# Optimization experiments

Measured on AMD Instinct MI355X. Metric: run time of the kernel, lower is better.

Reference implementation:

```python
import jax, jax.numpy as jnp
import numpy as np


def setup_inputs() -> dict:
    key = jax.random.key(0)
    k1, k2, k3, k4, k5 = jax.random.split(key, 5)
    B, N, T, O, G = 32, 256, 1024, 1024, 8
    x = jax.random.normal(k1, (B, N, T), dtype=jnp.float32)
    y = jax.random.uniform(k2, (B, G), dtype=jnp.float32)  # genre mixture weights
    weight = jax.random.normal(k3, (G, O, T), dtype=jnp.float32) * (1.0 / np.sqrt(T))
    mask = jax.random.uniform(k4, (O, T), dtype=jnp.float32)
    bias = jax.random.normal(k5, (O,), dtype=jnp.float32)
    return {"x": x, "y": y, "weight": weight, "mask": mask, "bias": bias}


def reference(x, y, weight, mask, bias):
    # mask the shared weight bank: [G,O,T] * [1,O,T]
    masked_w = weight * mask[None, :, :]
    # per-sample genre-mixed weights: [B,G] x [G,O,T] -> [B,O,T]
    w_bot = jnp.einsum('bg,got->bot', y, masked_w)
    # batched masked linear: [B,N,T] x [B,O,T] -> [B,N,O], plus bias
    return jnp.einsum('bnt,bot->bno', x, w_bot) + bias
```

## Files before the change

### kernel.cpp

```cpp
#include <hip/hip_runtime.h>
#include <hip/hip_bf16.h>
#include <stdint.h>


#define B_ 32
#define N_ 256
#define T_ 1024
#define O_ 1024
#define G_ 8

#define WSTRIDE ((size_t)(O_ * T_ + 2048))

#define BM 128
#define BN 128
#define BK 64
#define BUFSZ (BM * BK)

typedef __attribute__((__ext_vector_type__(8)))  __bf16 bf16x8;
typedef __attribute__((__ext_vector_type__(16))) float  f32x16;

__device__ __forceinline__ unsigned short f2bf(float f) {
    union { float f; uint32_t u; } v; v.f = f;
    uint32_t u = v.u;
    uint32_t r = (u + 0x7fffu + ((u >> 16) & 1u)) >> 16;
    return (unsigned short)r;
}

__device__ __forceinline__ uint4 pack8(const float* a) {
    uint4 r;
    r.x = (uint32_t)f2bf(a[0]) | ((uint32_t)f2bf(a[1]) << 16);
    r.y = (uint32_t)f2bf(a[2]) | ((uint32_t)f2bf(a[3]) << 16);
    r.z = (uint32_t)f2bf(a[4]) | ((uint32_t)f2bf(a[5]) << 16);
    r.w = (uint32_t)f2bf(a[6]) | ((uint32_t)f2bf(a[7]) << 16);
    return r;
}

#define MIXB 1024
#define CVTB 1024

__global__ __launch_bounds__(256) void prep_kernel(
    const float* __restrict__ w,
    const float* __restrict__ mask,
    const float* __restrict__ y,
    const float* __restrict__ x,
    unsigned short* __restrict__ Wb,
    unsigned short* __restrict__ xb)
{
    const int tid = threadIdx.x;
    if (blockIdx.x < MIXB) {
        const int idx = blockIdx.x * 256 + tid;
        const int o   = idx >> 8;
        const int t   = (idx & 255) << 2;

        const float4 m4 = *(const float4*)(mask + (size_t)o * T_ + t);

        float wv[G_][4];
#pragma unroll
        for (int g = 0; g < G_; ++g) {
            const float4 a = *(const float4*)(w + ((size_t)g * O_ + o) * T_ + t);
            wv[g][0] = a.x * m4.x; wv[g][1] = a.y * m4.y;
            wv[g][2] = a.z * m4.z; wv[g][3] = a.w * m4.w;
        }
        unsigned short* dst = Wb + (size_t)o * T_ + t;
        const int bph = blockIdx.x & (B_ - 1);
#pragma unroll 4
        for (int bi = 0; bi < B_; ++bi) {
            const int b = (bi + bph) & (B_ - 1);
            const float4 y0 = *(const float4*)(y + b * G_);
            const float4 y1 = *(const float4*)(y + b * G_ + 4);
            const float yv[G_] = {y0.x, y0.y, y0.z, y0.w, y1.x, y1.y, y1.z, y1.w};
            float acc[4] = {};
#pragma unroll
            for (int g = 0; g < G_; ++g)
#pragma unroll
                for (int j = 0; j < 4; ++j)
                    acc[j] += yv[g] * wv[g][j];
            ushort4 pk;
            pk.x = f2bf(acc[0]); pk.y = f2bf(acc[1]);
            pk.z = f2bf(acc[2]); pk.w = f2bf(acc[3]);
            *(ushort4*)(dst + (size_t)b * WSTRIDE) = pk;
        }
    } else {
        const int i = (blockIdx.x - MIXB) * 256 + tid;
        const float4* x4 = (const float4*)x;
        uint4* o4 = (uint4*)xb;
#pragma unroll
        for (int j = 0; j < 4; ++j) {
            const size_t f4 = (size_t)j * 524288 + (size_t)i * 2;
            const float4 a = x4[f4];
            const float4 b = x4[f4 + 1];
            const float v[8] = {a.x, a.y, a.z, a.w, b.x, b.y, b.z, b.w};
            o4[(size_t)j * 262144 + i] = pack8(v);
        }
    }
}

__device__ __forceinline__ void load16_to_lds(const unsigned short* g, unsigned short* l) {
    __builtin_amdgcn_global_load_lds(
        (const __attribute__((address_space(1))) unsigned char*)g,
        (__attribute__((address_space(3))) unsigned char*)l,
        16, 0, 0);
}

__global__ __launch_bounds__(256, 2) void gemm_kernel(
    const unsigned short* __restrict__ xb,
    const unsigned short* __restrict__ Wb,
    const float* __restrict__ bias,
    float* __restrict__ out)
{
    __shared__ __align__(16) unsigned short lA[2 * BUFSZ];
    __shared__ __align__(16) unsigned short lB[2 * BUFSZ];

    const int tn = blockIdx.x;
    const int tm = blockIdx.y;
    const int b  = blockIdx.z;

    const int tid  = threadIdx.x;
    const int lane = tid & 63;
    const int wave = tid >> 6;
    const int wm   = (wave >> 1) * 64;
    const int wn   = (wave & 1) * 64;

    const unsigned short* Ab = xb + (size_t)b * N_ * T_ + (size_t)(tm * BM) * T_;
    const unsigned short* Bb = Wb + (size_t)b * WSTRIDE + (size_t)(tn * BN) * T_;

    const int srow   = tid >> 3;
    const int schunk = (tid & 7) ^ (srow & 7);
    const unsigned short* ga0 = Ab + (size_t)srow * T_ + schunk * 8;
    const unsigned short* gb0 = Bb + (size_t)srow * T_ + schunk * 8;

#define STAGE(buf, kt)                                                          \
    {                                                                           \
        unsigned short* lad = lA + (buf) * BUFSZ + tid * 8;                     \
        unsigned short* lbd = lB + (buf) * BUFSZ + tid * 8;                     \
        _Pragma("unroll")                                                       \
        for (int i_ = 0; i_ < 4; ++i_) {                                        \
            load16_to_lds(ga0 + (kt) + (size_t)(i_ * 32) * T_, lad + i_ * 2048);\
            load16_to_lds(gb0 + (kt) + (size_t)(i_ * 32) * T_, lbd + i_ * 2048);\
        }                                                                       \
    }

    f32x16 acc[2][2] = {};

    const int fr   = lane & 31;
    const int half = lane >> 5;
    const int sw   = fr & 7;

#define COMPUTE(buf)                                                            \
    {                                                                           \
        const unsigned short* la = lA + (buf) * BUFSZ;                          \
        const unsigned short* lb = lB + (buf) * BUFSZ;                          \
        _Pragma("unroll")                                                       \
        for (int ks = 0; ks < 4; ++ks) {                                        \
            const int cp = (((ks * 2 + half)) ^ sw) * 8;                        \
            bf16x8 afr[2], bfr[2];                                              \
            _Pragma("unroll")                                                   \
            for (int i_ = 0; i_ < 2; ++i_)                                      \
                afr[i_] = *(const bf16x8*)(la + (wm + i_ * 32 + fr) * BK + cp); \
            _Pragma("unroll")                                                   \
            for (int i_ = 0; i_ < 2; ++i_)                                      \
                bfr[i_] = *(const bf16x8*)(lb + (wn + i_ * 32 + fr) * BK + cp); \
            _Pragma("unroll")                                                   \
            for (int mi = 0; mi < 2; ++mi)                                      \
                _Pragma("unroll")                                               \
                for (int ni = 0; ni < 2; ++ni)                                  \
                    acc[mi][ni] = __builtin_amdgcn_mfma_f32_32x32x16_bf16(      \
                        afr[mi], bfr[ni], acc[mi][ni], 0, 0, 0);                \
        }                                                                       \
    }

    STAGE(0, 0)
    for (int kt = 0; kt < T_; kt += 2 * BK) {
        __syncthreads();
        STAGE(1, kt + BK)
        COMPUTE(0)
        __syncthreads();
        if (kt + 2 * BK < T_) STAGE(0, kt + 2 * BK)
        COMPUTE(1)
    }

    float* outb = out + (size_t)b * N_ * O_ + (size_t)(tm * BM) * O_ + (tn * BN);
    const int cn = lane & 31;
    const int rb = (lane >> 5) * 4;
#pragma unroll
    for (int ni = 0; ni < 2; ++ni) {
        const int col = wn + ni * 32 + cn;
        const float bv = bias[tn * BN + col];
#pragma unroll
        for (int mi = 0; mi < 2; ++mi) {
#pragma unroll
            for (int r = 0; r < 16; ++r) {
                const int row = wm + mi * 32 + rb + (r & 3) + 8 * (r >> 2);
                outb[(size_t)row * O_ + col] = acc[mi][ni][r] + bv;
            }
        }
    }
}

__global__ __launch_bounds__(256) void naive_kernel(
    const float* __restrict__ x, const float* __restrict__ y,
    const float* __restrict__ w, const float* __restrict__ mask,
    const float* __restrict__ bias, float* __restrict__ out)
{
    const int oc = blockIdx.x & 3;
    const int n  = (blockIdx.x >> 2) & (N_ - 1);
    const int b  = blockIdx.x >> 10;

    __shared__ float xs[T_];
    __shared__ float ys[G_];
    const float* xrow = x + ((size_t)b * N_ + n) * T_;
    for (int i = threadIdx.x; i < T_ / 4; i += 256)
        ((float4*)xs)[i] = ((const float4*)xrow)[i];
    if (threadIdx.x < G_) ys[threadIdx.x] = y[b * G_ + threadIdx.x];
    __syncthreads();

    const int o = oc * 256 + threadIdx.x;
    float acc = 0.f;
    for (int t = 0; t < T_; t += 4) {
        const float4 m4 = *(const float4*)(mask + (size_t)o * T_ + t);
        float4 s = {0.f, 0.f, 0.f, 0.f};
#pragma unroll
        for (int g = 0; g < G_; ++g) {
            const float4 w4 = *(const float4*)(w + ((size_t)g * O_ + o) * T_ + t);
            const float yv = ys[g];
            s.x += yv * w4.x; s.y += yv * w4.y; s.z += yv * w4.z; s.w += yv * w4.w;
        }
        acc += xs[t] * m4.x * s.x + xs[t + 1] * m4.y * s.y
             + xs[t + 2] * m4.z * s.z + xs[t + 3] * m4.w * s.w;
    }
    out[((size_t)b * N_ + n) * O_ + o] = acc + bias[o];
}

extern "C" void kernel_launch(void* const* d_in, const int* in_sizes, int n_in,
                              void* d_out, int out_size, void* d_ws, size_t ws_size,
                              hipStream_t stream) {
    const float* x    = (const float*)d_in[0];
    const float* y    = (const float*)d_in[1];
    const float* w    = (const float*)d_in[2];
    const float* mask = (const float*)d_in[3];
    const float* bias = (const float*)d_in[4];
    float* out = (float*)d_out;

    const size_t wb_bytes = (size_t)B_ * WSTRIDE * sizeof(unsigned short);
    const size_t xb_bytes = (size_t)B_ * N_ * T_ * sizeof(unsigned short);

    if (ws_size >= wb_bytes + xb_bytes) {
        unsigned short* Wb = (unsigned short*)d_ws;
        unsigned short* xb = (unsigned short*)((char*)d_ws + wb_bytes);
        prep_kernel<<<MIXB + CVTB, 256, 0, stream>>>(w, mask, y, x, Wb, xb);
        dim3 grid(O_ / BN, N_ / BM, B_);
        gemm_kernel<<<grid, 256, 0, stream>>>(xb, Wb, bias, out);
    } else {
        naive_kernel<<<B_ * N_ * (O_ / 256), 256, 0, stream>>>(x, y, w, mask, bias, out);
    }
}
```

Before: 158.9 us.

## Fuse genre weight mixing and masking into GEMM tile loading

Removes the precomputed per-batch bf16 weight buffer and instead mixes the eight genre weights, applies the mask, and converts to bf16 directly into shared memory inside the GEMM loop. Tiles change to 256x64 with one block per (batch, output tile), and the x conversion becomes a separate small kernel. This avoids writing and rereading a large mixed-weight workspace. In exchange it gives up double buffering, rereads the fp32 weight bank per batch, and adds mixing arithmetic to the main loop.

```diff
diff --git a/kernel.cpp b/kernel.cpp
--- a/kernel.cpp
+++ b/kernel.cpp
@@ -9,12 +9,9 @@
 #define O_ 1024
 #define G_ 8
 
-#define WSTRIDE ((size_t)(O_ * T_ + 2048))
-
-#define BM 128
-#define BN 128
+#define BM 256
+#define BN 64
 #define BK 64
-#define BUFSZ (BM * BK)
 
 typedef __attribute__((__ext_vector_type__(8)))  __bf16 bf16x8;
 typedef __attribute__((__ext_vector_type__(16))) float  f32x16;
@@ -35,63 +32,21 @@
     return r;
 }
 
-#define MIXB 1024
 #define CVTB 1024
 
-__global__ __launch_bounds__(256) void prep_kernel(
-    const float* __restrict__ w,
-    const float* __restrict__ mask,
-    const float* __restrict__ y,
-    const float* __restrict__ x,
-    unsigned short* __restrict__ Wb,
-    unsigned short* __restrict__ xb)
+__global__ __launch_bounds__(256) void cvt_kernel(
+    const float* __restrict__ x, unsigned short* __restrict__ xb)
 {
-    const int tid = threadIdx.x;
-    if (blockIdx.x < MIXB) {
-        const int idx = blockIdx.x * 256 + tid;
-        const int o   = idx >> 8;
-        const int t   = (idx & 255) << 2;
-
-        const float4 m4 = *(const float4*)(mask + (size_t)o * T_ + t);
-
-        float wv[G_][4];
-#pragma unroll
-        for (int g = 0; g < G_; ++g) {
-            const float4 a = *(const float4*)(w + ((size_t)g * O_ + o) * T_ + t);
-            wv[g][0] = a.x * m4.x; wv[g][1] = a.y * m4.y;
-            wv[g][2] = a.z * m4.z; wv[g][3] = a.w * m4.w;
-        }
-        unsigned short* dst = Wb + (size_t)o * T_ + t;
-        const int bph = blockIdx.x & (B_ - 1);
-#pragma unroll 4
-        for (int bi = 0; bi < B_; ++bi) {
-            const int b = (bi + bph) & (B_ - 1);
-            const float4 y0 = *(const float4*)(y + b * G_);
-            const float4 y1 = *(const float4*)(y + b * G_ + 4);
-            const float yv[G_] = {y0.x, y0.y, y0.z, y0.w, y1.x, y1.y, y1.z, y1.w};
-            float acc[4] = {};
-#pragma unroll
-            for (int g = 0; g < G_; ++g)
-#pragma unroll
-                for (int j = 0; j < 4; ++j)
-                    acc[j] += yv[g] * wv[g][j];
-            ushort4 pk;
-            pk.x = f2bf(acc[0]); pk.y = f2bf(acc[1]);
-            pk.z = f2bf(acc[2]); pk.w = f2bf(acc[3]);
-            *(ushort4*)(dst + (size_t)b * WSTRIDE) = pk;
-        }
-    } else {
-        const int i = (blockIdx.x - MIXB) * 256 + tid;
-        const float4* x4 = (const float4*)x;
-        uint4* o4 = (uint4*)xb;
-#pragma unroll
-        for (int j = 0; j < 4; ++j) {
-            const size_t f4 = (size_t)j * 524288 + (size_t)i * 2;
-            const float4 a = x4[f4];
-            const float4 b = x4[f4 + 1];
-            const float v[8] = {a.x, a.y, a.z, a.w, b.x, b.y, b.z, b.w};
-            o4[(size_t)j * 262144 + i] = pack8(v);
-        }
+    const int i = blockIdx.x * 256 + threadIdx.x;
+    const float4* x4 = (const float4*)x;
+    uint4* o4 = (uint4*)xb;
+#pragma unroll
+    for (int j = 0; j < 4; ++j) {
+        const size_t f4 = (size_t)j * 524288 + (size_t)i * 2;
+        const float4 a = x4[f4];
+        const float4 b = x4[f4 + 1];
+        const float v[8] = {a.x, a.y, a.z, a.w, b.x, b.y, b.z, b.w};
+        o4[(size_t)j * 262144 + i] = pack8(v);
     }
 }
 
@@ -102,43 +57,39 @@
         16, 0, 0);
 }
 
-__global__ __launch_bounds__(256, 2) void gemm_kernel(
+__global__ __launch_bounds__(256, 2) void fused_kernel(
     const unsigned short* __restrict__ xb,
-    const unsigned short* __restrict__ Wb,
+    const float* __restrict__ w,
+    const float* __restrict__ mask,
+    const float* __restrict__ y,
     const float* __restrict__ bias,
     float* __restrict__ out)
 {
-    __shared__ __align__(16) unsigned short lA[2 * BUFSZ];
-    __shared__ __align__(16) unsigned short lB[2 * BUFSZ];
-
-    const int tn = blockIdx.x;
-    const int tm = blockIdx.y;
-    const int b  = blockIdx.z;
+    __shared__ __align__(16) unsigned short lA[BM * BK];
+    __shared__ __align__(16) unsigned short lB[BN * BK];
+
+    const int bx = blockIdx.x;
+    const int ot = bx & 15;
+    const int b  = bx >> 4;
 
     const int tid  = threadIdx.x;
     const int lane = tid & 63;
     const int wave = tid >> 6;
-    const int wm   = (wave >> 1) * 64;
-    const int wn   = (wave & 1) * 64;
-
-    const unsigned short* Ab = xb + (size_t)b * N_ * T_ + (size_t)(tm * BM) * T_;
-    const unsigned short* Bb = Wb + (size_t)b * WSTRIDE + (size_t)(tn * BN) * T_;
+    const int wm   = wave * 64;
 
     const int srow   = tid >> 3;
     const int schunk = (tid & 7) ^ (srow & 7);
-    const unsigned short* ga0 = Ab + (size_t)srow * T_ + schunk * 8;
-    const unsigned short* gb0 = Bb + (size_t)srow * T_ + schunk * 8;
-
-#define STAGE(buf, kt)                                                          \
-    {                                                                           \
-        unsigned short* lad = lA + (buf) * BUFSZ + tid * 8;                     \
-        unsigned short* lbd = lB + (buf) * BUFSZ + tid * 8;                     \
-        _Pragma("unroll")                                                       \
-        for (int i_ = 0; i_ < 4; ++i_) {                                        \
-            load16_to_lds(ga0 + (kt) + (size_t)(i_ * 32) * T_, lad + i_ * 2048);\
-            load16_to_lds(gb0 + (kt) + (size_t)(i_ * 32) * T_, lbd + i_ * 2048);\
-        }                                                                       \
-    }
+    const unsigned short* gA =
+        xb + (size_t)b * N_ * T_ + (size_t)srow * T_ + schunk * 8;
+
+    const int mr  = tid >> 2;
+    const int mcp = tid & 3;
+    const int mo  = ot * BN + mr;
+    const float* mp  = mask + (size_t)mo * T_;
+    const float* wp0 = w + (size_t)mo * T_;
+    float yv[G_];
+#pragma unroll
+    for (int g = 0; g < G_; ++g) yv[g] = y[b * G_ + g];
 
     f32x16 acc[2][2] = {};
 
@@ -146,46 +97,63 @@
     const int half = lane >> 5;
     const int sw   = fr & 7;
 
-#define COMPUTE(buf)                                                            \
-    {                                                                           \
-        const unsigned short* la = lA + (buf) * BUFSZ;                          \
-        const unsigned short* lb = lB + (buf) * BUFSZ;                          \
-        _Pragma("unroll")                                                       \
-        for (int ks = 0; ks < 4; ++ks) {                                        \
-            const int cp = (((ks * 2 + half)) ^ sw) * 8;                        \
-            bf16x8 afr[2], bfr[2];                                              \
-            _Pragma("unroll")                                                   \
-            for (int i_ = 0; i_ < 2; ++i_)                                      \
-                afr[i_] = *(const bf16x8*)(la + (wm + i_ * 32 + fr) * BK + cp); \
-            _Pragma("unroll")                                                   \
-            for (int i_ = 0; i_ < 2; ++i_)                                      \
-                bfr[i_] = *(const bf16x8*)(lb + (wn + i_ * 32 + fr) * BK + cp); \
-            _Pragma("unroll")                                                   \
-            for (int mi = 0; mi < 2; ++mi)                                      \
-                _Pragma("unroll")                                               \
-                for (int ni = 0; ni < 2; ++ni)                                  \
-                    acc[mi][ni] = __builtin_amdgcn_mfma_f32_32x32x16_bf16(      \
-                        afr[mi], bfr[ni], acc[mi][ni], 0, 0, 0);                \
-        }                                                                       \
-    }
-
-    STAGE(0, 0)
-    for (int kt = 0; kt < T_; kt += 2 * BK) {
+    for (int kt = 0; kt < T_; kt += BK) {
+#pragma unroll
+        for (int r8 = 0; r8 < 8; ++r8)
+            load16_to_lds(gA + kt + (size_t)(r8 * 32) * T_, lA + tid * 8 + r8 * 2048);
+
+#pragma unroll
+        for (int cc = 0; cc < 2; ++cc) {
+            const int c  = 2 * mcp + cc;
+            const int gk = kt + c * 8;
+            const float4 ma = *(const float4*)(mp + gk);
+            const float4 mb = *(const float4*)(mp + gk + 4);
+            float a8[8] = {};
+#pragma unroll
+            for (int g = 0; g < G_; ++g) {
+                const float* wp = wp0 + (size_t)g * O_ * T_ + gk;
+                const float4 wa = *(const float4*)(wp);
+                const float4 wb = *(const float4*)(wp + 4);
+                a8[0] += yv[g] * wa.x; a8[1] += yv[g] * wa.y;
+                a8[2] += yv[g] * wa.z; a8[3] += yv[g] * wa.w;
+                a8[4] += yv[g] * wb.x; a8[5] += yv[g] * wb.y;
+                a8[6] += yv[g] * wb.z; a8[7] += yv[g] * wb.w;
+            }
+            a8[0] *= ma.x; a8[1] *= ma.y; a8[2] *= ma.z; a8[3] *= ma.w;
+            a8[4] *= mb.x; a8[5] *= mb.y; a8[6] *= mb.z; a8[7] *= mb.w;
+            *(uint4*)(lB + mr * BK + ((c ^ (mr & 7)) * 8)) = pack8(a8);
+        }
+
         __syncthreads();
-        STAGE(1, kt + BK)
-        COMPUTE(0)
+
+#pragma unroll
+        for (int ks = 0; ks < 4; ++ks) {
+            const int cp = ((ks * 2 + half) ^ sw) * 8;
+            bf16x8 afr[2], bfr[2];
+#pragma unroll
+            for (int i_ = 0; i_ < 2; ++i_)
+                afr[i_] = *(const bf16x8*)(lA + (wm + i_ * 32 + fr) * BK + cp);
+#pragma unroll
+            for (int i_ = 0; i_ < 2; ++i_)
+                bfr[i_] = *(const bf16x8*)(lB + (i_ * 32 + fr) * BK + cp);
+#pragma unroll
+            for (int mi = 0; mi < 2; ++mi)
+#pragma unroll
+                for (int ni = 0; ni < 2; ++ni)
+                    acc[mi][ni] = __builtin_amdgcn_mfma_f32_32x32x16_bf16(
+                        afr[mi], bfr[ni], acc[mi][ni], 0, 0, 0);
+        }
+
         __syncthreads();
-        if (kt + 2 * BK < T_) STAGE(0, kt + 2 * BK)
-        COMPUTE(1)
-    }
-
-    float* outb = out + (size_t)b * N_ * O_ + (size_t)(tm * BM) * O_ + (tn * BN);
+    }
+
+    float* outb = out + (size_t)b * N_ * O_ + (ot * BN);
     const int cn = lane & 31;
     const int rb = (lane >> 5) * 4;
 #pragma unroll
     for (int ni = 0; ni < 2; ++ni) {
-        const int col = wn + ni * 32 + cn;
-        const float bv = bias[tn * BN + col];
+        const int col = ni * 32 + cn;
+        const float bv = bias[ot * BN + col];
 #pragma unroll
         for (int mi = 0; mi < 2; ++mi) {
 #pragma unroll
@@ -241,15 +209,12 @@
     const float* bias = (const float*)d_in[4];
     float* out = (float*)d_out;
 
-    const size_t wb_bytes = (size_t)B_ * WSTRIDE * sizeof(unsigned short);
     const size_t xb_bytes = (size_t)B_ * N_ * T_ * sizeof(unsigned short);
 
-    if (ws_size >= wb_bytes + xb_bytes) {
-        unsigned short* Wb = (unsigned short*)d_ws;
-        unsigned short* xb = (unsigned short*)((char*)d_ws + wb_bytes);
-        prep_kernel<<<MIXB + CVTB, 256, 0, stream>>>(w, mask, y, x, Wb, xb);
-        dim3 grid(O_ / BN, N_ / BM, B_);
-        gemm_kernel<<<grid, 256, 0, stream>>>(xb, Wb, bias, out);
+    if (ws_size >= xb_bytes) {
+        unsigned short* xb = (unsigned short*)d_ws;
+        cvt_kernel<<<CVTB, 256, 0, stream>>>(x, xb);
+        fused_kernel<<<(O_ / BN) * B_, 256, 0, stream>>>(xb, w, mask, y, bias, out);
     } else {
         naive_kernel<<<B_ * N_ * (O_ / 256), 256, 0, stream>>>(x, y, w, mask, bias, out);
     }
```

Result: slower. 213.5 us (+34.3%).
